# Optimization experiments

Measured on AMD Instinct MI355X. Metric: run time of the kernel, lower is better.

Reference implementation:

```python
import jax, jax.numpy as jnp
import numpy as np

N = 12288       # tree nodes
V = 1000        # wordpiece vocab (len(char_list))
EMBDIM = 256    # embdim
EMBSIZE = 32    # embsize (GCN hidden)


def setup_inputs() -> dict:
    key = jax.random.key(0)
    k1, k2, k3, k4 = jax.random.split(key, 4)
    node_ids = jax.random.randint(k1, (N,), 0, V)

    # Build a random prefix-tree topology: parent[i] < i for i >= 1.
    rng = np.random.default_rng(0)
    parents = (rng.random(N - 1) * np.arange(1, N)).astype(np.int64)
    children = np.arange(1, N, dtype=np.int64)
    self_loops = np.stack([np.arange(N, dtype=np.int64)] * 2, axis=1)   # [N,2]
    pc = np.stack([parents, children], axis=1)                           # [N-1,2]
    edges = jnp.asarray(np.concatenate([self_loops, pc], axis=0))        # [2N-1,2]

    embed_table = jax.random.normal(k2, (V, EMBDIM), dtype=jnp.float32) * 0.02
    W1 = jax.random.normal(k3, (EMBDIM, EMBSIZE), dtype=jnp.float32) / np.sqrt(EMBDIM)
    b1 = jnp.zeros((EMBSIZE,), dtype=jnp.float32)
    W2 = jax.random.normal(k4, (EMBSIZE, EMBSIZE), dtype=jnp.float32) / np.sqrt(EMBSIZE)
    b2 = jnp.zeros((EMBSIZE,), dtype=jnp.float32)
    return {"node_ids": node_ids, "edges": edges, "embed_table": embed_table,
            "W1": W1, "b1": b1, "W2": W2, "b2": b2}


def reference(node_ids, edges, embed_table, W1, b1, W2, b2):
    # Embedding gather for every tree node (dropout is identity at eval).
    emb = embed_table[node_ids]                                   # [N, EMBDIM]
    # Dense adjacency from edge list: self-loops + parent->child (directed).
    A = jnp.zeros((N, N), dtype=embed_table.dtype)
    A = A.at[edges[:, 0], edges[:, 1]].set(1.0)
    # Symmetric degree normalization D^{-1/2} A D^{-1/2} (degrees = row sums).
    d = jnp.sum(A, axis=-1) ** -0.5                               # rows have >=1 (self-loop)
    A_norm = d[:, None] * A * d[None, :]
    # Two-layer GCN.
    h = jax.nn.relu(A_norm @ (emb @ W1 + b1))                     # [N, EMBSIZE]
    h = jax.nn.relu(A_norm @ (h @ W2 + b2))                       # [N, EMBSIZE]
    return h
```

## Files before the change

kernel.cpp:

```cpp
#include <hip/hip_runtime.h>
#include <hip/hip_bf16.h>

#define NN 12288
#define ED 256
#define ES 32
#define NPC (NN - 1)
#define BLK 256

typedef __hip_bfloat16 bf16;
typedef __attribute__((ext_vector_type(8))) short s8v;
typedef __attribute__((ext_vector_type(8))) unsigned short u8v;
typedef __attribute__((ext_vector_type(4))) float f4v;

__device__ __forceinline__ bool detect_f32(const void* W1) {
    const unsigned short* p = (const unsigned short*)W1 + (threadIdx.x & 63) * 8;
    u8v v = *(const u8v*)p;
    int huge = 0;
#pragma unroll
    for (int i = 0; i < 8; ++i) {
        unsigned short m = (unsigned short)(v[i] & 0x7fff);
        huge |= (m >= 0x4620);
    }
    return __any(huge) != 0;
}

__device__ __forceinline__ float ldv(const void* p, int i, bool f32) {
    return f32 ? ((const float*)p)[i] : __bfloat162float(((const bf16*)p)[i]);
}

__device__ __forceinline__ unsigned short f2bf(float f) {
    bf16 h = __float2bfloat16(f);
    return __builtin_bit_cast(unsigned short, h);
}

__global__ __launch_bounds__(BLK)
void k1(const int* __restrict__ node_ids, const int* __restrict__ edges,
        const void* __restrict__ table, const void* __restrict__ W1,
        const void* __restrict__ b1, unsigned* __restrict__ deg,
        float* __restrict__ X) {
    __shared__ unsigned short sW1T[ES * ED];
    bool f32 = detect_f32(W1);
    int tt = threadIdx.x;
    unsigned t = blockIdx.x * BLK + tt;
    if (t < NPC) atomicAdd(&deg[edges[2 * (NN + t)]], 1u);

    {
        int j = tt & 31, kc = tt >> 5;
        for (int it = 0; it < 4; ++it) {
            int kb = kc + 8 * it;
            u8v v;
            if (f32) {
                const float* w = (const float*)W1;
#pragma unroll
                for (int e = 0; e < 8; ++e) v[e] = f2bf(w[(kb * 8 + e) * ES + j]);
            } else {
                const unsigned short* w = (const unsigned short*)W1;
#pragma unroll
                for (int e = 0; e < 8; ++e) v[e] = w[(kb * 8 + e) * ES + j];
            }
            *(u8v*)&sW1T[j * ED + ((kb ^ (j & 7)) * 8)] = v;
        }
    }
    __syncthreads();

    int lane = tt & 63;
    int q = lane & 15, hi = lane >> 4;
    int n0 = blockIdx.x * 64 + (tt >> 6) * 16;
    size_t id = (size_t)node_ids[n0 + q];
    f4v a0 = {0.f, 0.f, 0.f, 0.f}, a1 = {0.f, 0.f, 0.f, 0.f};
    int sw = q & 7;
    if (f32) {
        const float* e = (const float*)table + id * ED + hi * 8;
#pragma unroll
        for (int s = 0; s < 8; ++s) {
            f4v e0 = *(const f4v*)(e + s * 32);
            f4v e1 = *(const f4v*)(e + s * 32 + 4);
            u8v av;
#pragma unroll
            for (int i = 0; i < 4; ++i) { av[i] = f2bf(e0[i]); av[4 + i] = f2bf(e1[i]); }
            int blk = (hi + 4 * s) ^ sw;
            s8v b0  = *(const s8v*)&sW1T[q * ED + blk * 8];
            s8v b1v = *(const s8v*)&sW1T[(q + 16) * ED + blk * 8];
            s8v a = __builtin_bit_cast(s8v, av);
            a0 = __builtin_amdgcn_mfma_f32_16x16x32_bf16(a, b0,  a0, 0, 0, 0);
            a1 = __builtin_amdgcn_mfma_f32_16x16x32_bf16(a, b1v, a1, 0, 0, 0);
        }
    } else {
        const short* e = (const short*)table + id * ED + hi * 8;
#pragma unroll
        for (int s = 0; s < 8; ++s) {
            s8v a = *(const s8v*)(e + s * 32);
            int blk = (hi + 4 * s) ^ sw;
            s8v b0  = *(const s8v*)&sW1T[q * ED + blk * 8];
            s8v b1v = *(const s8v*)&sW1T[(q + 16) * ED + blk * 8];
            a0 = __builtin_amdgcn_mfma_f32_16x16x32_bf16(a, b0,  a0, 0, 0, 0);
            a1 = __builtin_amdgcn_mfma_f32_16x16x32_bf16(a, b1v, a1, 0, 0, 0);
        }
    }
    float bv0 = ldv(b1, q, f32), bv1 = ldv(b1, q + 16, f32);
#pragma unroll
    for (int i = 0; i < 4; ++i) {
        int n = n0 + hi * 4 + i;
        X[n * ES + q]      = a0[i] + bv0;
        X[n * ES + q + 16] = a1[i] + bv1;
    }
}

__global__ __launch_bounds__(BLK)
void k2(const int* __restrict__ edges, const unsigned* __restrict__ deg,
        const float* __restrict__ X, float* __restrict__ acc1) {
    unsigned t = blockIdx.x * BLK + threadIdx.x;
    if (t >= (unsigned)NPC * ES) return;
    int e = t >> 5, k = t & 31;
    int c = e + 1;
    int r = edges[2 * (NN + e)];
    float w = rsqrtf((float)deg[r] + 1.f) * rsqrtf((float)deg[c] + 1.f);
    atomicAdd(&acc1[r * ES + k], w * X[c * ES + k]);
}

__global__ __launch_bounds__(BLK)
void k3(const int* __restrict__ edges, const void* __restrict__ W1,
        const void* __restrict__ W2, const void* __restrict__ b2,
        const unsigned* __restrict__ deg, const float* __restrict__ acc1,
        const float* __restrict__ X, float* __restrict__ acc2) {
    __shared__ float sW2[ES * 33];
    __shared__ float sB[ES];
    bool f32 = detect_f32(W1);
    int tt = threadIdx.x;
    for (int i = tt; i < ES * ES; i += BLK) sW2[(i >> 5) * 33 + (i & 31)] = ldv(W2, i, f32);
    if (tt < ES) sB[tt] = ldv(b2, tt, f32);
    __syncthreads();
    unsigned t = blockIdx.x * BLK + tt;
    if (t >= (unsigned)NPC * ES) return;
    int e = t >> 5, j = t & 31;
    int c = e + 1;
    int r = edges[2 * (NN + e)];
    float rc = rsqrtf((float)deg[c] + 1.f);
    float h = fmaxf(acc1[c * ES + j] + (rc * rc) * X[c * ES + j], 0.f);
    float x2 = sB[j];
    #pragma unroll
    for (int k = 0; k < ES; ++k)
        x2 += __shfl(h, k, ES) * sW2[k * 33 + j];
    float w = rsqrtf((float)deg[r] + 1.f) * rc;
    atomicAdd(&acc2[r * ES + j], w * x2);
}

__global__ __launch_bounds__(BLK)
void k4(const void* __restrict__ W1, const void* __restrict__ W2,
        const void* __restrict__ b2, const unsigned* __restrict__ deg,
        const float* __restrict__ acc1, const float* __restrict__ X,
        const float* __restrict__ acc2, void* __restrict__ out) {
    __shared__ float sW2[ES * 33];
    __shared__ float sB[ES];
    bool f32 = detect_f32(W1);
    int tt = threadIdx.x;
    for (int i = tt; i < ES * ES; i += BLK) sW2[(i >> 5) * 33 + (i & 31)] = ldv(W2, i, f32);
    if (tt < ES) sB[tt] = ldv(b2, tt, f32);
    __syncthreads();
    unsigned t = blockIdx.x * BLK + tt;
    int n = t >> 5, j = t & 31;
    float rn = rsqrtf((float)deg[n] + 1.f);
    float sw = rn * rn;
    float h = fmaxf(acc1[n * ES + j] + sw * X[n * ES + j], 0.f);
    float x2 = sB[j];
    #pragma unroll
    for (int k = 0; k < ES; ++k)
        x2 += __shfl(h, k, ES) * sW2[k * 33 + j];
    float v = fmaxf(acc2[n * ES + j] + sw * x2, 0.f);
    if (f32) ((float*)out)[t] = v;
    else     ((bf16*)out)[t]  = __float2bfloat16(v);
}

extern "C" void kernel_launch(void* const* d_in, const int* in_sizes, int n_in,
                              void* d_out, int out_size, void* d_ws, size_t ws_size,
                              hipStream_t stream) {
    const int* node_ids = (const int*)d_in[0];
    const int* edges    = (const int*)d_in[1];
    const void* table   = d_in[2];
    const void* W1      = d_in[3];
    const void* b1      = d_in[4];
    const void* W2      = d_in[5];
    const void* b2      = d_in[6];

    char* ws = (char*)d_ws;
    unsigned* deg = (unsigned*)ws;
    float* acc1   = (float*)(ws + (size_t)NN * 4);
    float* acc2   = acc1 + (size_t)NN * ES;
    float* X      = acc2 + (size_t)NN * ES;

    hipMemsetAsync(d_ws, 0, (size_t)NN * 4 + 2ull * NN * ES * 4, stream);

    const int g_mfma = NN / 64;
    const int g_node = NN * ES / BLK;
    const int g_edge = (NPC * ES + BLK - 1) / BLK;

    k1<<<g_mfma, BLK, 0, stream>>>(node_ids, edges, table, W1, b1, deg, X);
    k2<<<g_edge, BLK, 0, stream>>>(edges, deg, X, acc1);
    k3<<<g_edge, BLK, 0, stream>>>(edges, W1, W2, b2, deg, acc1, X, acc2);
    k4<<<g_node, BLK, 0, stream>>>(W1, W2, b2, deg, acc1, X, acc2, d_out);
}
```

Baseline: 88.30 us.

## Precompute degrees in a zeroing kernel and fuse first aggregation into embedding GEMM

Adds a k0 kernel where block 0 computes node degrees with shared-memory atomics while the other blocks zero the accumulators, replacing the memset. Because degrees are now known before k1 runs, k1 can scatter its X outputs into acc1 directly, which removes the separate k2 edge kernel and its reread of X. The cost is that one block handles all 12K degree atomics serially, and k1 now issues global atomics from its epilogue.

```diff
diff --git a/kernel.cpp b/kernel.cpp
--- a/kernel.cpp
+++ b/kernel.cpp
@@ -34,15 +34,33 @@
 }
 
 __global__ __launch_bounds__(BLK)
+void k0(const int* __restrict__ edges, unsigned* __restrict__ deg,
+        float4* __restrict__ accz) {
+    if (blockIdx.x == 0) {
+        __shared__ unsigned sdeg[NN];
+        int tt = threadIdx.x;
+        for (int i = tt; i < NN; i += BLK) sdeg[i] = 0u;
+        __syncthreads();
+        for (int e = tt; e < NPC; e += BLK)
+            atomicAdd(&sdeg[edges[2 * (NN + e)]], 1u);
+        __syncthreads();
+        for (int i = tt; i < NN; i += BLK) deg[i] = sdeg[i];
+    } else {
+        const unsigned n4 = 2u * NN * ES / 4;
+        unsigned i = (blockIdx.x - 1) * BLK + threadIdx.x;
+        const unsigned stride = (gridDim.x - 1) * BLK;
+        for (; i < n4; i += stride) accz[i] = make_float4(0.f, 0.f, 0.f, 0.f);
+    }
+}
+
+__global__ __launch_bounds__(BLK)
 void k1(const int* __restrict__ node_ids, const int* __restrict__ edges,
         const void* __restrict__ table, const void* __restrict__ W1,
-        const void* __restrict__ b1, unsigned* __restrict__ deg,
-        float* __restrict__ X) {
+        const void* __restrict__ b1, const unsigned* __restrict__ deg,
+        float* __restrict__ X, float* __restrict__ acc1) {
     __shared__ unsigned short sW1T[ES * ED];
     bool f32 = detect_f32(W1);
     int tt = threadIdx.x;
-    unsigned t = blockIdx.x * BLK + tt;
-    if (t < NPC) atomicAdd(&deg[edges[2 * (NN + t)]], 1u);
 
     {
         int j = tt & 31, kc = tt >> 5;
@@ -101,21 +119,16 @@
 #pragma unroll
     for (int i = 0; i < 4; ++i) {
         int n = n0 + hi * 4 + i;
-        X[n * ES + q]      = a0[i] + bv0;
-        X[n * ES + q + 16] = a1[i] + bv1;
-    }
-}
-
-__global__ __launch_bounds__(BLK)
-void k2(const int* __restrict__ edges, const unsigned* __restrict__ deg,
-        const float* __restrict__ X, float* __restrict__ acc1) {
-    unsigned t = blockIdx.x * BLK + threadIdx.x;
-    if (t >= (unsigned)NPC * ES) return;
-    int e = t >> 5, k = t & 31;
-    int c = e + 1;
-    int r = edges[2 * (NN + e)];
-    float w = rsqrtf((float)deg[r] + 1.f) * rsqrtf((float)deg[c] + 1.f);
-    atomicAdd(&acc1[r * ES + k], w * X[c * ES + k]);
+        float x0 = a0[i] + bv0, x1 = a1[i] + bv1;
+        X[n * ES + q]      = x0;
+        X[n * ES + q + 16] = x1;
+        if (n > 0) {
+            int r = edges[2 * (NN + n - 1)];
+            float w = rsqrtf((float)deg[r] + 1.f) * rsqrtf((float)deg[n] + 1.f);
+            atomicAdd(&acc1[r * ES + q],      w * x0);
+            atomicAdd(&acc1[r * ES + q + 16], w * x1);
+        }
+    }
 }
 
 __global__ __launch_bounds__(BLK)
@@ -188,14 +201,12 @@
     float* acc2   = acc1 + (size_t)NN * ES;
     float* X      = acc2 + (size_t)NN * ES;
 
-    hipMemsetAsync(d_ws, 0, (size_t)NN * 4 + 2ull * NN * ES * 4, stream);
-
     const int g_mfma = NN / 64;
     const int g_node = NN * ES / BLK;
     const int g_edge = (NPC * ES + BLK - 1) / BLK;
 
-    k1<<<g_mfma, BLK, 0, stream>>>(node_ids, edges, table, W1, b1, deg, X);
-    k2<<<g_edge, BLK, 0, stream>>>(edges, deg, X, acc1);
+    k0<<<97,     BLK, 0, stream>>>(edges, deg, (float4*)acc1);
+    k1<<<g_mfma, BLK, 0, stream>>>(node_ids, edges, table, W1, b1, deg, X, acc1);
     k3<<<g_edge, BLK, 0, stream>>>(edges, W1, W2, b2, deg, acc1, X, acc2);
     k4<<<g_node, BLK, 0, stream>>>(W1, W2, b2, deg, acc1, X, acc2, d_out);
 }
```

Measured after the change: 100.5 us. 13.8% more time.

## Fuse workspace zeroing and degree counting into first kernel, drop memset

Applied to the files above, without the earlier changes.

Removes the separate memset launch by having the embedding/projection kernel zero the two accumulator buffers with float4 stores. Degree counting switches from global atomics to per-block LDS histograms, where each block scans all parent edges and keeps the counts for its own 64 nodes, then writes deg directly. This saves a launch and contention on global atomics. In exchange, every block re-reads the whole edge list, about 12K parent entries per block across 192 blocks.

```diff
diff --git a/kernel.cpp b/kernel.cpp
--- a/kernel.cpp
+++ b/kernel.cpp
@@ -37,12 +37,19 @@
 void k1(const int* __restrict__ node_ids, const int* __restrict__ edges,
         const void* __restrict__ table, const void* __restrict__ W1,
         const void* __restrict__ b1, unsigned* __restrict__ deg,
-        float* __restrict__ X) {
+        float* __restrict__ X, float4* __restrict__ accz) {
     __shared__ unsigned short sW1T[ES * ED];
+    __shared__ unsigned cnt[64];
     bool f32 = detect_f32(W1);
     int tt = threadIdx.x;
-    unsigned t = blockIdx.x * BLK + tt;
-    if (t < NPC) atomicAdd(&deg[edges[2 * (NN + t)]], 1u);
+    if (tt < 64) cnt[tt] = 0u;
+
+    {
+        unsigned tid = blockIdx.x * BLK + tt;
+        const unsigned n4 = 2u * NN * ES / 4;
+        for (unsigned i = tid; i < n4; i += 192u * BLK)
+            accz[i] = make_float4(0.f, 0.f, 0.f, 0.f);
+    }
 
     {
         int j = tt & 31, kc = tt >> 5;
@@ -62,6 +69,23 @@
         }
     }
     __syncthreads();
+
+    {
+        int lo = blockIdx.x * 64;
+        for (int base = 0; base < 48; base += 8) {
+            int pb[8];
+#pragma unroll
+            for (int u = 0; u < 8; ++u) {
+                int e = tt + (base + u) * BLK;
+                pb[u] = (e < NPC) ? edges[2 * (NN + e)] : -1;
+            }
+#pragma unroll
+            for (int u = 0; u < 8; ++u) {
+                int p = pb[u] - lo;
+                if (p >= 0 && p < 64) atomicAdd(&cnt[p], 1u);
+            }
+        }
+    }
 
     int lane = tt & 63;
     int q = lane & 15, hi = lane >> 4;
@@ -104,6 +128,9 @@
         X[n * ES + q]      = a0[i] + bv0;
         X[n * ES + q + 16] = a1[i] + bv1;
     }
+
+    __syncthreads();
+    if (tt < 64) deg[blockIdx.x * 64 + tt] = cnt[tt];
 }
 
 __global__ __launch_bounds__(BLK)
@@ -188,13 +215,11 @@
     float* acc2   = acc1 + (size_t)NN * ES;
     float* X      = acc2 + (size_t)NN * ES;
 
-    hipMemsetAsync(d_ws, 0, (size_t)NN * 4 + 2ull * NN * ES * 4, stream);
-
     const int g_mfma = NN / 64;
     const int g_node = NN * ES / BLK;
     const int g_edge = (NPC * ES + BLK - 1) / BLK;
 
-    k1<<<g_mfma, BLK, 0, stream>>>(node_ids, edges, table, W1, b1, deg, X);
+    k1<<<g_mfma, BLK, 0, stream>>>(node_ids, edges, table, W1, b1, deg, X, (float4*)acc1);
     k2<<<g_edge, BLK, 0, stream>>>(edges, deg, X, acc1);
     k3<<<g_edge, BLK, 0, stream>>>(edges, W1, W2, b2, deg, acc1, X, acc2);
     k4<<<g_node, BLK, 0, stream>>>(W1, W2, b2, deg, acc1, X, acc2, d_out);
```

Result: no change. 89.47 us (+1.3%).
